# Kernel optimization log

Hardware: AMD Instinct MI355X
Metric: run time of the kernel (lower is better)

Reference implementation:

```python
import jax, jax.numpy as jnp
import numpy as np

N_HEADS = 8
NS = 4  # samples per point


def _ref_grid(H, W):
    # matches torch: pts[i,j] = ((i+0.5)/(H-1), (j+0.5)/(W-1)) * 2 - 1  -> (y, x)
    ys = ((jnp.arange(H, dtype=jnp.float32) + 0.5) / (H - 1)) * 2.0 - 1.0
    xs = ((jnp.arange(W, dtype=jnp.float32) + 0.5) / (W - 1)) * 2.0 - 1.0
    ref = jnp.stack(jnp.meshgrid(ys, xs, indexing='ij'), axis=-1)  # [H,W,2]
    return ref.reshape(H * W, 2)


def _bilinear_sample(img_flat, yx, H, W):
    # img_flat: [D, H*W], yx: [L, n, 2] normalized (y,x) in [-1,1]
    # grid_sample(mode='bilinear', padding_mode='zeros', align_corners=True)
    y = (yx[..., 0] + 1.0) * 0.5 * (H - 1)
    x = (yx[..., 1] + 1.0) * 0.5 * (W - 1)
    y0 = jnp.floor(y)
    x0 = jnp.floor(x)
    out = jnp.zeros((img_flat.shape[0],) + y.shape, dtype=img_flat.dtype)
    for dy in (0.0, 1.0):
        for dx in (0.0, 1.0):
            yi = y0 + dy
            xi = x0 + dx
            w = (1.0 - jnp.abs(y - yi)) * (1.0 - jnp.abs(x - xi))
            valid = (yi >= 0) & (yi < H) & (xi >= 0) & (xi < W)
            yc = jnp.clip(yi, 0, H - 1).astype(jnp.int32)
            xc = jnp.clip(xi, 0, W - 1).astype(jnp.int32)
            idx = yc * W + xc  # [L,n]
            vals = jnp.take(img_flat, idx.reshape(-1), axis=1).reshape(
                img_flat.shape[0], *idx.shape)  # [D,L,n]
            out = out + vals * jnp.where(valid, w, 0.0)[None]
    return out  # [D,L,n]


def setup_inputs() -> dict:
    key = jax.random.key(0)
    ks = jax.random.split(key, 9)
    B, C, H, W = 8, 256, 64, 64
    A, N = N_HEADS, NS
    x = jax.random.normal(ks[0], (B, C, H, W), dtype=jnp.float32)
    w_att = jax.random.normal(ks[1], (A * N, C), dtype=jnp.float32) * 0.02
    b_att = jnp.zeros((A * N,), dtype=jnp.float32)
    w_off = jax.random.normal(ks[2], (A * N * 2, C), dtype=jnp.float32) * 0.01
    b_off = jax.random.normal(ks[3], (A * N * 2,), dtype=jnp.float32) * 0.1
    w_v = jax.random.normal(ks[4], (C, C), dtype=jnp.float32) * 0.02
    b_v = jnp.zeros((C,), dtype=jnp.float32)
    w_out = jax.random.normal(ks[5], (C, C), dtype=jnp.float32) * 0.02
    b_out = jnp.zeros((C,), dtype=jnp.float32)
    return {"x": x, "w_att": w_att, "b_att": b_att, "w_off": w_off,
            "b_off": b_off, "w_v": w_v, "b_v": b_v, "w_out": w_out,
            "b_out": b_out}


def reference(x, w_att, b_att, w_off, b_off, w_v, b_v, w_out, b_out):
    B, C, H, W = x.shape
    A, N = N_HEADS, NS
    D = C // A
    L = H * W
    xl = x.reshape(B, C, L).transpose(0, 2, 1)  # [B,L,C]
    attn = jax.nn.softmax((xl @ w_att.T + b_att).reshape(B, L, A, N), axis=-1)
    off = (xl @ w_off.T + b_off).reshape(B, L, A, N, 2)
    ref = _ref_grid(H, W)  # [L,2] (y,x)
    pos = ref[None, :, None, None, :] + off  # [B,L,A,N,2]
    pos = pos.transpose(0, 2, 1, 3, 4).reshape(B * A, L, N, 2)
    v = jnp.einsum('bchw,oc->bohw', x, w_v) + b_v[None, :, None, None]
    v_flat = v.reshape(B * A, D, L)
    samp = jax.vmap(lambda im, g: _bilinear_sample(im, g, H, W))(v_flat, pos)  # [BA,D,L,N]
    attn_ = attn.transpose(0, 2, 1, 3).reshape(B * A, L, N)
    agg = (samp * attn_[:, None]).sum(axis=3)  # [BA,D,L]
    v2 = agg.reshape(B, A * D, H, W)
    y = jnp.einsum('bchw,oc->bohw', v2, w_out) + b_out[None, :, None, None]
    return y
```

## Files before the change

kernel.cpp:

```cpp
#include <hip/hip_runtime.h>
#include <math.h>
#include <stdint.h>

#define BQ 8
#define CC 256
#define HH 64
#define WW 64
#define LL 4096
#define AH 8
#define DD 32

typedef __attribute__((ext_vector_type(4))) float f32x4;
typedef __attribute__((ext_vector_type(8))) short short8;

__device__ __forceinline__ uint32_t pk_bf16(float a, float b) {
    uint32_t r;
    asm("v_cvt_pk_bf16_f32 %0, %1, %2" : "=v"(r) : "v"(a), "v"(b));
    return r;
}
__device__ __forceinline__ float bf_lo(uint32_t u) { return __uint_as_float(u << 16); }
__device__ __forceinline__ float bf_hi(uint32_t u) { return __uint_as_float(u & 0xffff0000u); }

__device__ __forceinline__ void split2(float a, float b, uint32_t& hi, uint32_t& lo) {
    hi = pk_bf16(a, b);
    float ah = bf_lo(hi), bh = bf_hi(hi);
    lo = pk_bf16(a - ah, b - bh);
}


__device__ __forceinline__ void load8(float4 v[8], const float* p, size_t stride) {
#pragma unroll
    for (int i = 0; i < 8; ++i) v[i] = *(const float4*)(p + (size_t)i * stride);
}

__device__ __forceinline__ void writeA(const float4 av[8], uint32_t* as, int a_r0, int a_f4) {
#pragma unroll
    for (int i = 0; i < 8; ++i) {
        int r = a_r0 + i * 16;
        uint32_t lo = pk_bf16(av[i].x, av[i].y);
        uint32_t hi = pk_bf16(av[i].z, av[i].w);
        int slot = (a_f4 >> 1) ^ (r & 7);
        *(uint2*)&as[r * 32 + (slot << 2) + ((a_f4 & 1) << 1)] = make_uint2(lo, hi);
    }
}

__device__ __forceinline__ void writeB_x(const float4 bv[8], uint32_t* bs, int b_kb, int b_l0) {
#pragma unroll
    for (int j = 0; j < 4; ++j) {
        int l = b_l0 * 4 + j;
        uint32_t w0 = pk_bf16(((const float*)&bv[0])[j], ((const float*)&bv[1])[j]);
        uint32_t w1 = pk_bf16(((const float*)&bv[2])[j], ((const float*)&bv[3])[j]);
        uint32_t w2 = pk_bf16(((const float*)&bv[4])[j], ((const float*)&bv[5])[j]);
        uint32_t w3 = pk_bf16(((const float*)&bv[6])[j], ((const float*)&bv[7])[j]);
        int slot = b_kb ^ (l & 7);
        *(uint4*)&bs[l * 32 + (slot << 2)] = make_uint4(w0, w1, w2, w3);
    }
}

__device__ __forceinline__ void compute_tile(const uint32_t* as, const uint32_t* bs,
                                             f32x4 acc[4][4], int lane, int wm, int wn) {
#pragma unroll
    for (int ks = 0; ks < 2; ++ks) {
        int ag = ks * 4 + (lane >> 4);
        short8 af[4], bf[4];
#pragma unroll
        for (int mf = 0; mf < 4; ++mf) {
            int r = wm * 64 + mf * 16 + (lane & 15);
            af[mf] = *(const short8*)&as[r * 32 + ((ag ^ (r & 7)) << 2)];
        }
#pragma unroll
        for (int nf = 0; nf < 4; ++nf) {
            int r = wn * 64 + nf * 16 + (lane & 15);
            bf[nf] = *(const short8*)&bs[r * 32 + ((ag ^ (r & 7)) << 2)];
        }
#pragma unroll
        for (int mf = 0; mf < 4; ++mf)
#pragma unroll
            for (int nf = 0; nf < 4; ++nf)
                acc[mf][nf] = __builtin_amdgcn_mfma_f32_16x16x32_bf16(
                    af[mf], bf[nf], acc[mf][nf], 0, 0, 0);
    }
}

__global__ __launch_bounds__(256)
void pack_wout(const float* __restrict__ Wm, uint32_t* __restrict__ w_pack)
{
    int id = blockIdx.x * 256 + threadIdx.x;
    int lane  = id & 63;
    int kc    = (id >> 6) & 7;
    int otile = id >> 9;
    int o  = otile * 16 + (lane & 15);
    int k0 = kc * 32 + (lane >> 4) * 8;
    const float* wp = Wm + (size_t)o * CC + k0;
    float4 v0 = *(const float4*)wp;
    float4 v1 = *(const float4*)(wp + 4);
    ((uint4*)w_pack)[id] = make_uint4(pk_bf16(v0.x, v0.y), pk_bf16(v0.z, v0.w),
                                      pk_bf16(v1.x, v1.y), pk_bf16(v1.z, v1.w));
}

__global__ __launch_bounds__(256, 2)
void gemm_attoff(const float* __restrict__ X,
                 const float* __restrict__ w_att, const float* __restrict__ w_off,
                 const float* __restrict__ b_att, const float* __restrict__ b_off,
                 float* __restrict__ outbuf)
{
    __shared__ uint32_t ah_s[2][96 * 32];
    __shared__ uint32_t al_s[2][96 * 32];
    __shared__ uint32_t bh_s[2][64 * 32];
    __shared__ uint32_t bl_s[2][64 * 32];

    const int lb = blockIdx.x;
    const int b  = blockIdx.y;
    const int t  = threadIdx.x;
    const int lane = t & 63;
    const int wv = t >> 6;
    const int wm = wv >> 1, wn = wv & 1;

    const int tr   = t >> 4;
    const int a_f4 = t & 15;
    const int b_kb = t & 7;
    const int b_l0 = t >> 3;

    const float* Bp = X + ((size_t)b * CC + b_kb * 8) * LL + lb * 64 + b_l0 * 2;

    f32x4 acc[3][2];
#pragma unroll
    for (int i = 0; i < 3; ++i)
#pragma unroll
        for (int j = 0; j < 2; ++j) acc[i][j] = (f32x4)0.0f;

    float4 av[6];
    float2 bv[8];

    auto loadT = [&](int kc) {
#pragma unroll
        for (int i = 0; i < 6; ++i) {
            int r = i * 16 + tr;
            const float* wp = (i < 2) ? (w_att + (size_t)r * CC)
                                      : (w_off + (size_t)(r - 32) * CC);
            av[i] = *(const float4*)(wp + kc * 64 + a_f4 * 4);
        }
#pragma unroll
        for (int m = 0; m < 8; ++m)
            bv[m] = *(const float2*)(Bp + (size_t)(kc * 64 + m) * LL);
    };

    auto writeT = [&](int buf) {
#pragma unroll
        for (int i = 0; i < 6; ++i) {
            int r = i * 16 + tr;
            uint32_t h0, q0, h1, q1;
            split2(av[i].x, av[i].y, h0, q0);
            split2(av[i].z, av[i].w, h1, q1);
            int idx = r * 32 + (((a_f4 >> 1) ^ (r & 7)) << 2) + ((a_f4 & 1) << 1);
            *(uint2*)&ah_s[buf][idx] = make_uint2(h0, h1);
            *(uint2*)&al_s[buf][idx] = make_uint2(q0, q1);
        }
#pragma unroll
        for (int j = 0; j < 2; ++j) {
            int l = b_l0 * 2 + j;
            uint32_t h[4], q[4];
#pragma unroll
            for (int p = 0; p < 4; ++p) {
                float e0 = j ? bv[2 * p].y     : bv[2 * p].x;
                float e1 = j ? bv[2 * p + 1].y : bv[2 * p + 1].x;
                split2(e0, e1, h[p], q[p]);
            }
            int idx = l * 32 + ((b_kb ^ (l & 7)) << 2);
            *(uint4*)&bh_s[buf][idx] = make_uint4(h[0], h[1], h[2], h[3]);
            *(uint4*)&bl_s[buf][idx] = make_uint4(q[0], q[1], q[2], q[3]);
        }
    };

    auto computeT = [&](int buf) {
#pragma unroll
        for (int ks = 0; ks < 2; ++ks) {
            int ag = ks * 4 + (lane >> 4);
            short8 afh[3], afl[3], bfh[2], bfl[2];
#pragma unroll
            for (int mf = 0; mf < 3; ++mf) {
                int r = wm * 48 + mf * 16 + (lane & 15);
                int off = r * 32 + ((ag ^ (r & 7)) << 2);
                afh[mf] = *(const short8*)&ah_s[buf][off];
                afl[mf] = *(const short8*)&al_s[buf][off];
            }
#pragma unroll
            for (int nf = 0; nf < 2; ++nf) {
                int r = wn * 32 + nf * 16 + (lane & 15);
                int off = r * 32 + ((ag ^ (r & 7)) << 2);
                bfh[nf] = *(const short8*)&bh_s[buf][off];
                bfl[nf] = *(const short8*)&bl_s[buf][off];
            }
#pragma unroll
            for (int mf = 0; mf < 3; ++mf)
#pragma unroll
                for (int nf = 0; nf < 2; ++nf) {
                    acc[mf][nf] = __builtin_amdgcn_mfma_f32_16x16x32_bf16(
                        afh[mf], bfh[nf], acc[mf][nf], 0, 0, 0);
                    acc[mf][nf] = __builtin_amdgcn_mfma_f32_16x16x32_bf16(
                        afh[mf], bfl[nf], acc[mf][nf], 0, 0, 0);
                    acc[mf][nf] = __builtin_amdgcn_mfma_f32_16x16x32_bf16(
                        afl[mf], bfh[nf], acc[mf][nf], 0, 0, 0);
                }
        }
    };

    loadT(0);
    writeT(0);
    __syncthreads();
    for (int kc = 0; kc < 4; ++kc) {
        const int cur = kc & 1;
        if (kc < 3) loadT(kc + 1);
        computeT(cur);
        if (kc < 3) { writeT(cur ^ 1); __syncthreads(); }
    }

    const int l_base = lb * 64 + wn * 32 + (lane & 15);
    const int o_base = wm * 48 + ((lane >> 4) << 2);
#pragma unroll
    for (int mf = 0; mf < 3; ++mf) {
        int o0 = o_base + mf * 16;
        const float* bp = (o0 < 32) ? (b_att + o0) : (b_off + (o0 - 32));
        float4 bs = *(const float4*)bp;
#pragma unroll
        for (int nf = 0; nf < 2; ++nf) {
            int l = l_base + nf * 16;
            float* op = outbuf + ((size_t)b * 96 + o0) * LL + l;
            op[(size_t)0 * LL] = acc[mf][nf][0] + bs.x;
            op[(size_t)1 * LL] = acc[mf][nf][1] + bs.y;
            op[(size_t)2 * LL] = acc[mf][nf][2] + bs.z;
            op[(size_t)3 * LL] = acc[mf][nf][3] + bs.w;
        }
    }
}

__global__ __launch_bounds__(256, 2)
void gemm_v(const float* __restrict__ X, const float* __restrict__ Wm,
            const float* __restrict__ bias, uint16_t* __restrict__ vout)
{
    __shared__ uint32_t a_s[2][128 * 32];
    __shared__ uint32_t b_s[2][128 * 32];

    const int nb = blockIdx.x;
    const int b  = nb >> 5;
    const int lb = nb & 31;
    const int ob = blockIdx.y;
    const int t  = threadIdx.x;
    const int lane = t & 63;
    const int wv = t >> 6;
    const int wm = wv >> 1, wn = wv & 1;

    const int a_f4 = t & 15, a_r0 = t >> 4;
    const int b_kb = t & 7,  b_l0 = t >> 3;

    const float* Ap = Wm + (size_t)(ob * 128 + a_r0) * CC + a_f4 * 4;
    const float* Bp = X + ((size_t)b * CC + b_kb * 8) * LL + lb * 128 + b_l0 * 4;

    f32x4 acc[4][4];
#pragma unroll
    for (int i = 0; i < 4; ++i)
#pragma unroll
        for (int j = 0; j < 4; ++j) acc[i][j] = (f32x4)0.0f;

    float4 av[8], bv[8];
    load8(av, Ap, (size_t)16 * CC);
    load8(bv, Bp, (size_t)LL);
    writeA(av, a_s[0], a_r0, a_f4);
    writeB_x(bv, b_s[0], b_kb, b_l0);
    __syncthreads();

    for (int kc = 0; kc < 4; ++kc) {
        const int cur = kc & 1;
        if (kc < 3) {
            load8(av, Ap + (kc + 1) * 64, (size_t)16 * CC);
            load8(bv, Bp + (size_t)(kc + 1) * 64 * LL, (size_t)LL);
        }
        compute_tile(a_s[cur], b_s[cur], acc, lane, wm, wn);
        if (kc < 3) {
            writeA(av, a_s[cur ^ 1], a_r0, a_f4);
            writeB_x(bv, b_s[cur ^ 1], b_kb, b_l0);
            __syncthreads();
        }
    }

    const int l_base = lb * 128 + wn * 64 + (lane & 15);
    const int o_base = ob * 128 + wm * 64 + ((lane >> 4) << 2);
#pragma unroll
    for (int mf = 0; mf < 4; ++mf) {
        int o0 = o_base + mf * 16;
        float4 bs = *(const float4*)(bias + o0);
        int a_h = o0 >> 5;
        int d0 = o0 & 31;
#pragma unroll
        for (int nf = 0; nf < 4; ++nf) {
            int l = l_base + nf * 16;
            uint32_t p0 = pk_bf16(acc[mf][nf][0] + bs.x, acc[mf][nf][1] + bs.y);
            uint32_t p1 = pk_bf16(acc[mf][nf][2] + bs.z, acc[mf][nf][3] + bs.w);
            *(uint2*)(vout + ((size_t)(b * AH + a_h) * LL + l) * DD + d0) =
                make_uint2(p0, p1);
        }
    }
}

__global__ __launch_bounds__(256, 2)
void sample_out(const uint16_t* __restrict__ v_samp,
                const float* __restrict__ logits,
                const uint32_t* __restrict__ w_pack,
                const float* __restrict__ bias,
                float* __restrict__ out)
{
    __shared__ uint32_t agg_s[64 * 128];

    const int bid = blockIdx.x;
    const int b   = bid & 7;
    const int lt  = bid >> 3;
    const int t   = threadIdx.x;
    const int lane = t & 63;
    const int wv  = t >> 6;

    const int l_loc = t & 63;
    const int l = lt * 64 + l_loc;
    const int gi = l >> 6, gj = l & 63;
    const float ry = (gi + 0.5f) * (2.0f / 63.0f) - 1.0f;
    const float rx = (gj + 0.5f) * (2.0f / 63.0f) - 1.0f;

#pragma unroll
    for (int hh = 0; hh < 2; ++hh) {
        const int a = (t >> 6) + hh * 4;

        const float* la = logits + ((size_t)b * 96 + a * 4) * LL + l;
        float e0 = la[0], e1 = la[(size_t)LL], e2 = la[(size_t)2 * LL], e3 = la[(size_t)3 * LL];
        float m = fmaxf(fmaxf(e0, e1), fmaxf(e2, e3));
        e0 = expf(e0 - m); e1 = expf(e1 - m); e2 = expf(e2 - m); e3 = expf(e3 - m);
        float inv = 1.0f / (e0 + e1 + e2 + e3);
        float attn[4] = {e0 * inv, e1 * inv, e2 * inv, e3 * inv};

        const float* lo = logits + ((size_t)b * 96 + 32 + a * 8) * LL + l;
        float pyy[4], pxx[4];
#pragma unroll
        for (int n = 0; n < 4; ++n) {
            pyy[n] = ry + lo[(size_t)(n * 2 + 0) * LL];
            pxx[n] = rx + lo[(size_t)(n * 2 + 1) * LL];
        }

        float acc[32];
#pragma unroll
        for (int q = 0; q < 32; ++q) acc[q] = 0.f;

        const uint16_t* vb = v_samp + (size_t)(b * AH + a) * LL * DD;
#pragma unroll
        for (int n = 0; n < 4; ++n) {
            float y = (pyy[n] + 1.0f) * 0.5f * 63.0f;
            float x = (pxx[n] + 1.0f) * 0.5f * 63.0f;
            float yf = floorf(y), xf = floorf(x);
            int y0i = (int)yf, x0i = (int)xf;
            float fy = y - yf, fx = x - xf;
            float wts[4] = {(1.f - fy) * (1.f - fx), (1.f - fy) * fx,
                            fy * (1.f - fx),         fy * fx};
            int yy[4] = {y0i, y0i, y0i + 1, y0i + 1};
            int xx[4] = {x0i, x0i + 1, x0i, x0i + 1};
#pragma unroll
            for (int c2 = 0; c2 < 4; ++c2) {
                int yc = yy[c2], xc = xx[c2];
                if (yc >= 0 && yc < HH && xc >= 0 && xc < WW) {
                    float w = attn[n] * wts[c2];
                    const uint4* vp = (const uint4*)(vb + (size_t)(yc * WW + xc) * DD);
#pragma unroll
                    for (int u = 0; u < 4; ++u) {
                        uint4 rv = vp[u];
                        acc[u * 8 + 0] += w * bf_lo(rv.x);
                        acc[u * 8 + 1] += w * bf_hi(rv.x);
                        acc[u * 8 + 2] += w * bf_lo(rv.y);
                        acc[u * 8 + 3] += w * bf_hi(rv.y);
                        acc[u * 8 + 4] += w * bf_lo(rv.z);
                        acc[u * 8 + 5] += w * bf_hi(rv.z);
                        acc[u * 8 + 6] += w * bf_lo(rv.w);
                        acc[u * 8 + 7] += w * bf_hi(rv.w);
                    }
                }
            }
        }
#pragma unroll
        for (int j = 0; j < 4; ++j) {
            int slot = (a * 4 + j) ^ (l_loc & 7);
            uint32_t p0 = pk_bf16(acc[j * 8 + 0], acc[j * 8 + 1]);
            uint32_t p1 = pk_bf16(acc[j * 8 + 2], acc[j * 8 + 3]);
            uint32_t p2 = pk_bf16(acc[j * 8 + 4], acc[j * 8 + 5]);
            uint32_t p3 = pk_bf16(acc[j * 8 + 6], acc[j * 8 + 7]);
            *(uint4*)&agg_s[l_loc * 128 + (slot << 2)] = make_uint4(p0, p1, p2, p3);
        }
    }
    __syncthreads();

    f32x4 acc2[4][4];
#pragma unroll
    for (int i = 0; i < 4; ++i)
#pragma unroll
        for (int j = 0; j < 4; ++j) acc2[i][j] = (f32x4)0.0f;

    for (int kc = 0; kc < 8; ++kc) {
        short8 af[4], bf[4];
#pragma unroll
        for (int mf = 0; mf < 4; ++mf) {
            int otile = wv * 4 + mf;
            af[mf] = *(const short8*)&w_pack[(size_t)((otile * 8 + kc) * 64 + lane) * 4];
        }
#pragma unroll
        for (int nf = 0; nf < 4; ++nf) {
            int r = nf * 16 + (lane & 15);
            int slot = kc * 4 + (lane >> 4);
            bf[nf] = *(const short8*)&agg_s[r * 128 + ((slot ^ (r & 7)) << 2)];
        }
#pragma unroll
        for (int mf = 0; mf < 4; ++mf)
#pragma unroll
            for (int nf = 0; nf < 4; ++nf)
                acc2[mf][nf] = __builtin_amdgcn_mfma_f32_16x16x32_bf16(
                    af[mf], bf[nf], acc2[mf][nf], 0, 0, 0);
    }

#pragma unroll
    for (int mf = 0; mf < 4; ++mf) {
        int o0 = wv * 64 + mf * 16 + ((lane >> 4) << 2);
        float4 bs = *(const float4*)(bias + o0);
#pragma unroll
        for (int nf = 0; nf < 4; ++nf) {
            int lx = lt * 64 + nf * 16 + (lane & 15);
            float* op = out + ((size_t)b * CC + o0) * LL + lx;
            op[(size_t)0 * LL] = acc2[mf][nf][0] + bs.x;
            op[(size_t)1 * LL] = acc2[mf][nf][1] + bs.y;
            op[(size_t)2 * LL] = acc2[mf][nf][2] + bs.z;
            op[(size_t)3 * LL] = acc2[mf][nf][3] + bs.w;
        }
    }
}

extern "C" void kernel_launch(void* const* d_in, const int* in_sizes, int n_in,
                              void* d_out, int out_size, void* d_ws, size_t ws_size,
                              hipStream_t stream) {
    const float* x     = (const float*)d_in[0];
    const float* w_att = (const float*)d_in[1];
    const float* b_att = (const float*)d_in[2];
    const float* w_off = (const float*)d_in[3];
    const float* b_off = (const float*)d_in[4];
    const float* w_v   = (const float*)d_in[5];
    const float* b_v   = (const float*)d_in[6];
    const float* w_out = (const float*)d_in[7];
    const float* b_out = (const float*)d_in[8];
    float* out = (float*)d_out;

    float* ws        = (float*)d_ws;
    float* logits    = ws;
    uint16_t* v_samp = (uint16_t*)(logits + (size_t)BQ * 96 * LL);
    uint32_t* w_pack = (uint32_t*)(v_samp + (size_t)BQ * AH * LL * DD);

    dim3 blk(256);
    pack_wout<<<dim3(32), blk, 0, stream>>>(w_out, w_pack);
    gemm_attoff<<<dim3(64, BQ), blk, 0, stream>>>(x, w_att, w_off, b_att, b_off, logits);
    gemm_v<<<dim3(256, 2), blk, 0, stream>>>(x, w_v, b_v, v_samp);
    sample_out<<<dim3(512), blk, 0, stream>>>(v_samp, logits, w_pack, b_out, out);
}
```

Before: 68.88 us.

## Split sampling channels across 4 threads per point and halve the tile

The sampling stage now assigns four threads per query point, each owning 8 of the 32 head channels, in place of one thread gathering all 32 channels. The tile shrinks to 32 points per block with a 1024-block grid, smaller shared memory and a 4-block launch bound. The aim is to cut per-thread register pressure, raise occupancy and make gathers more parallel to hide latency. In exchange, the softmax and offset logit loads are repeated per channel group, and each block does half as many MFMA columns while reloading the same weight fragments, so weight traffic per output rises.

```diff
diff --git a/kernel.cpp b/kernel.cpp
--- a/kernel.cpp
+++ b/kernel.cpp
@@ -302,14 +302,14 @@
     }
 }
 
-__global__ __launch_bounds__(256, 2)
+__global__ __launch_bounds__(256, 4)
 void sample_out(const uint16_t* __restrict__ v_samp,
                 const float* __restrict__ logits,
                 const uint32_t* __restrict__ w_pack,
                 const float* __restrict__ bias,
                 float* __restrict__ out)
 {
-    __shared__ uint32_t agg_s[64 * 128];
+    __shared__ uint32_t agg_s[32 * 128];
 
     const int bid = blockIdx.x;
     const int b   = bid & 7;
@@ -318,15 +318,17 @@
     const int lane = t & 63;
     const int wv  = t >> 6;
 
-    const int l_loc = t & 63;
-    const int l = lt * 64 + l_loc;
+    const int hp = t >> 7;
+    const int pt = (t >> 2) & 31;
+    const int cg = t & 3;
+    const int l  = lt * 32 + pt;
     const int gi = l >> 6, gj = l & 63;
     const float ry = (gi + 0.5f) * (2.0f / 63.0f) - 1.0f;
     const float rx = (gj + 0.5f) * (2.0f / 63.0f) - 1.0f;
 
 #pragma unroll
-    for (int hh = 0; hh < 2; ++hh) {
-        const int a = (t >> 6) + hh * 4;
+    for (int hi = 0; hi < 4; ++hi) {
+        const int a = hp * 4 + hi;
 
         const float* la = logits + ((size_t)b * 96 + a * 4) * LL + l;
         float e0 = la[0], e1 = la[(size_t)LL], e2 = la[(size_t)2 * LL], e3 = la[(size_t)3 * LL];
@@ -343,11 +345,11 @@
             pxx[n] = rx + lo[(size_t)(n * 2 + 1) * LL];
         }
 
-        float acc[32];
-#pragma unroll
-        for (int q = 0; q < 32; ++q) acc[q] = 0.f;
-
-        const uint16_t* vb = v_samp + (size_t)(b * AH + a) * LL * DD;
+        float acc[8];
+#pragma unroll
+        for (int q = 0; q < 8; ++q) acc[q] = 0.f;
+
+        const uint16_t* vb = v_samp + (size_t)(b * AH + a) * LL * DD + cg * 8;
 #pragma unroll
         for (int n = 0; n < 4; ++n) {
             float y = (pyy[n] + 1.0f) * 0.5f * 63.0f;
@@ -364,49 +366,39 @@
                 int yc = yy[c2], xc = xx[c2];
                 if (yc >= 0 && yc < HH && xc >= 0 && xc < WW) {
                     float w = attn[n] * wts[c2];
-                    const uint4* vp = (const uint4*)(vb + (size_t)(yc * WW + xc) * DD);
-#pragma unroll
-                    for (int u = 0; u < 4; ++u) {
-                        uint4 rv = vp[u];
-                        acc[u * 8 + 0] += w * bf_lo(rv.x);
-                        acc[u * 8 + 1] += w * bf_hi(rv.x);
-                        acc[u * 8 + 2] += w * bf_lo(rv.y);
-                        acc[u * 8 + 3] += w * bf_hi(rv.y);
-                        acc[u * 8 + 4] += w * bf_lo(rv.z);
-                        acc[u * 8 + 5] += w * bf_hi(rv.z);
-                        acc[u * 8 + 6] += w * bf_lo(rv.w);
-                        acc[u * 8 + 7] += w * bf_hi(rv.w);
-                    }
+                    uint4 rv = *(const uint4*)(vb + (size_t)(yc * WW + xc) * DD);
+                    acc[0] += w * bf_lo(rv.x); acc[1] += w * bf_hi(rv.x);
+                    acc[2] += w * bf_lo(rv.y); acc[3] += w * bf_hi(rv.y);
+                    acc[4] += w * bf_lo(rv.z); acc[5] += w * bf_hi(rv.z);
+                    acc[6] += w * bf_lo(rv.w); acc[7] += w * bf_hi(rv.w);
                 }
             }
         }
-#pragma unroll
-        for (int j = 0; j < 4; ++j) {
-            int slot = (a * 4 + j) ^ (l_loc & 7);
-            uint32_t p0 = pk_bf16(acc[j * 8 + 0], acc[j * 8 + 1]);
-            uint32_t p1 = pk_bf16(acc[j * 8 + 2], acc[j * 8 + 3]);
-            uint32_t p2 = pk_bf16(acc[j * 8 + 4], acc[j * 8 + 5]);
-            uint32_t p3 = pk_bf16(acc[j * 8 + 6], acc[j * 8 + 7]);
-            *(uint4*)&agg_s[l_loc * 128 + (slot << 2)] = make_uint4(p0, p1, p2, p3);
-        }
+        uint32_t p0 = pk_bf16(acc[0], acc[1]);
+        uint32_t p1 = pk_bf16(acc[2], acc[3]);
+        uint32_t p2 = pk_bf16(acc[4], acc[5]);
+        uint32_t p3 = pk_bf16(acc[6], acc[7]);
+        int sl = a * 4 + cg;
+        *(uint4*)&agg_s[pt * 128 + ((sl ^ (pt & 7)) << 2)] =
+            make_uint4(p0, p1, p2, p3);
     }
     __syncthreads();
 
-    f32x4 acc2[4][4];
+    f32x4 acc2[4][2];
 #pragma unroll
     for (int i = 0; i < 4; ++i)
 #pragma unroll
-        for (int j = 0; j < 4; ++j) acc2[i][j] = (f32x4)0.0f;
+        for (int j = 0; j < 2; ++j) acc2[i][j] = (f32x4)0.0f;
 
     for (int kc = 0; kc < 8; ++kc) {
-        short8 af[4], bf[4];
+        short8 af[4], bf[2];
 #pragma unroll
         for (int mf = 0; mf < 4; ++mf) {
             int otile = wv * 4 + mf;
             af[mf] = *(const short8*)&w_pack[(size_t)((otile * 8 + kc) * 64 + lane) * 4];
         }
 #pragma unroll
-        for (int nf = 0; nf < 4; ++nf) {
+        for (int nf = 0; nf < 2; ++nf) {
             int r = nf * 16 + (lane & 15);
             int slot = kc * 4 + (lane >> 4);
             bf[nf] = *(const short8*)&agg_s[r * 128 + ((slot ^ (r & 7)) << 2)];
@@ -414,7 +406,7 @@
 #pragma unroll
         for (int mf = 0; mf < 4; ++mf)
 #pragma unroll
-            for (int nf = 0; nf < 4; ++nf)
+            for (int nf = 0; nf < 2; ++nf)
                 acc2[mf][nf] = __builtin_amdgcn_mfma_f32_16x16x32_bf16(
                     af[mf], bf[nf], acc2[mf][nf], 0, 0, 0);
     }
@@ -424,8 +416,8 @@
         int o0 = wv * 64 + mf * 16 + ((lane >> 4) << 2);
         float4 bs = *(const float4*)(bias + o0);
 #pragma unroll
-        for (int nf = 0; nf < 4; ++nf) {
-            int lx = lt * 64 + nf * 16 + (lane & 15);
+        for (int nf = 0; nf < 2; ++nf) {
+            int lx = lt * 32 + nf * 16 + (lane & 15);
             float* op = out + ((size_t)b * CC + o0) * LL + lx;
             op[(size_t)0 * LL] = acc2[mf][nf][0] + bs.x;
             op[(size_t)1 * LL] = acc2[mf][nf][1] + bs.y;
@@ -458,5 +450,5 @@
     pack_wout<<<dim3(32), blk, 0, stream>>>(w_out, w_pack);
     gemm_attoff<<<dim3(64, BQ), blk, 0, stream>>>(x, w_att, w_off, b_att, b_off, logits);
     gemm_v<<<dim3(256, 2), blk, 0, stream>>>(x, w_v, b_v, v_samp);
-    sample_out<<<dim3(512), blk, 0, stream>>>(v_samp, logits, w_pack, b_out, out);
-}
+    sample_out<<<dim3(1024), blk, 0, stream>>>(v_samp, logits, w_pack, b_out, out);
+}
```

New measurement: 72.62 us. 1.05x slower.
